# Kernel tuning notes

Hardware: AMD Instinct MI355X
Metric: run time of the kernel (lower is better)

## Reference

```python
import jax, jax.numpy as jnp
import numpy as np

TWO_PI = 2.0 * np.pi
DT = 0.01            # self.dt buffer
COE_D, COE_M = 2, 8  # interp_degree, interp_mesh_size (per dim) for coe fitters
NL_D, NL_M = 4, 40   # nonlinear fitter degree / mesh_size
NL_A, NL_B = -15.0, 15.0  # nonlinear_interp_mesh_bound


def lagrange_basis(t, d):
    """Degree-d Lagrange basis at local coord t in [0,1]; returns [..., d+1]."""
    nodes = jnp.arange(d + 1, dtype=t.dtype) / d
    basis = []
    for j in range(d + 1):
        L = jnp.ones_like(t)
        for k in range(d + 1):
            if k != j:
                L = L * (t - nodes[k]) / (nodes[j] - nodes[k])
        basis.append(L)
    return jnp.stack(basis, axis=-1)


def interp_cells(x, a, b, m, d):
    """Map x to (cell index [..,], basis values [.., d+1]) on an m-cell mesh over [a,b]."""
    s = (x - a) / (b - a) * m
    cell = jnp.clip(jnp.floor(s), 0, m - 1)
    t = s - cell  # allows extrapolation outside [a,b] via edge cells
    return cell.astype(jnp.int32), lagrange_basis(t, d)


def nonlinear_interp(w, x):
    """1D piecewise-Lagrange fitter applied elementwise (nonlinearfitter)."""
    cell, L = interp_cells(x, NL_A, NL_B, NL_M, NL_D)
    idx = cell[..., None] * NL_D + jnp.arange(NL_D + 1)
    return jnp.sum(w[idx] * L, axis=-1)


def coe_fields(ws, xy):
    """2D tensor-product Lagrange interp on fixed inputs xy -> [C,H,W] coef fields."""
    c0, L0 = interp_cells(xy[..., 0], 0.0, TWO_PI, COE_M, COE_D)
    c1, L1 = interp_cells(xy[..., 1], 0.0, TWO_PI, COE_M, COE_D)
    i0 = c0[..., None] * COE_D + jnp.arange(COE_D + 1)   # [H,W,d+1]
    i1 = c1[..., None] * COE_D + jnp.arange(COE_D + 1)
    wloc = ws[:, i0[..., :, None], i1[..., None, :]]     # [C,H,W,d+1,d+1]
    return jnp.einsum('chwij,hwi,hwj->chw', wloc, L0, L1)


def conv_same(u, k):
    """u: [B,H,W], k: [N,1,kh,kw] -> [B,N,H,W] with zero (Dirichlet) padding."""
    return jax.lax.conv_general_dilated(u[:, None], k, (1, 1), 'SAME',
                                        dimension_numbers=('NCHW', 'OIHW', 'NCHW'))


def setup_inputs() -> dict:
    key = jax.random.key(0)
    ks = jax.random.split(key, 5)
    B, H, W, K, N = 16, 512, 512, 5, 6
    init = jax.random.normal(ks[0], (B, H, W), jnp.float32)
    delta = jnp.zeros((1, 1, K, K), jnp.float32).at[0, 0, K // 2, K // 2].set(1.0)
    idkernel = delta + 0.01 * jax.random.normal(ks[1], (1, 1, K, K), jnp.float32)
    fdkernel = 0.1 * jax.random.normal(ks[2], (N, 1, K, K), jnp.float32)
    M = COE_M * COE_D + 1
    coe_w = 0.1 * jax.random.normal(ks[3], (N - 1, M, M), jnp.float32)
    nl_w = 0.1 * jax.random.normal(ks[4], (NL_M * NL_D + 1,), jnp.float32)
    gx = jnp.linspace(0.0, TWO_PI, H, endpoint=False).astype(jnp.float32)
    xy = jnp.stack(jnp.meshgrid(gx, gx, indexing='ij'), axis=-1)  # [H,W,2]
    return {"init": init, "idkernel": idkernel, "fdkernel": fdkernel,
            "coe_w": coe_w, "nl_w": nl_w, "xy": xy, "stepnum": 8}


def reference(init, idkernel, fdkernel, coe_w, nl_w, xy, stepnum):
    # coefficient fields are evaluated once (fixed xy), as in the torch forward
    coe = coe_fields(coe_w, xy)[None]  # [1, N-1, H, W], broadcasts over batch

    def step(u, _):
        uid = conv_same(u, idkernel)[:, 0]           # [B,H,W]
        ufd = conv_same(u, fdkernel)                 # [B,N,H,W]
        un = uid + DT * ((coe * ufd[:, 1:]).sum(axis=1)
                         + nonlinear_interp(nl_w, ufd[:, 0]))
        return un, None

    u, _ = jax.lax.scan(step, init, None, length=stepnum)
    return u
```

## Files before the change

### kernel.cpp

```cpp
#include <hip/hip_runtime.h>

typedef float f2 __attribute__((ext_vector_type(2)));

static constexpr int HH = 512;
static constexpr int WW = 512;
static constexpr int NB = 16;
static constexpr float DT_F = 0.01f;
static constexpr float TWO_PI_F = 6.283185307179586f;
static constexpr int STEPS = 8;

static constexpr int TW = 64;
static constexpr int TH = 16;
static constexpr int LW = TW + 4;
static constexpr int LH = TH + 4;

__device__ const float NLM[5][5] = {
    {1.0f,      -25.0f/3.0f,   70.0f/3.0f,  -80.0f/3.0f,   32.0f/3.0f},
    {0.0f,       16.0f,      -208.0f/3.0f,   96.0f,      -128.0f/3.0f},
    {0.0f,      -12.0f,        76.0f,      -128.0f,        64.0f},
    {0.0f,   16.0f/3.0f,    -112.0f/3.0f,  224.0f/3.0f, -128.0f/3.0f},
    {0.0f,      -1.0f,       22.0f/3.0f,   -16.0f,        32.0f/3.0f},
};

__device__ __forceinline__ void pkfma_s(f2& acc, f2 w, f2 u) {
    asm("v_pk_fma_f32 %0, %1, %2, %0" : "+v"(acc) : "s"(w), "v"(u));
}
__device__ __forceinline__ void pkfma_v(f2& acc, f2 a, f2 b) {
    asm("v_pk_fma_f32 %0, %1, %2, %0" : "+v"(acc) : "v"(a), "v"(b));
}

__global__ __launch_bounds__(256) void coe_kernel(const float* __restrict__ coe_w,
                                                  const float* __restrict__ xy,
                                                  float* __restrict__ coe)
{
    __shared__ float sw[5 * 17 * 17];
    for (int i = threadIdx.x; i < 5 * 17 * 17; i += 256) sw[i] = coe_w[i];
    __syncthreads();

    int p = blockIdx.x * 256 + threadIdx.x;
    if (p >= HH * WW) return;

    float x0 = xy[2 * p + 0];
    float x1 = xy[2 * p + 1];

    float s0 = x0 / TWO_PI_F * 8.0f;
    float c0f = fminf(fmaxf(floorf(s0), 0.0f), 7.0f);
    float t0 = s0 - c0f;
    int i0 = 2 * (int)c0f;

    float s1 = x1 / TWO_PI_F * 8.0f;
    float c1f = fminf(fmaxf(floorf(s1), 0.0f), 7.0f);
    float t1 = s1 - c1f;
    int i1 = 2 * (int)c1f;

    float L0[3], L1[3];
    L0[0] = (t0 - 0.5f) * (t0 - 1.0f) * 2.0f;
    L0[1] = t0 * (t0 - 1.0f) * -4.0f;
    L0[2] = t0 * (t0 - 0.5f) * 2.0f;
    L1[0] = (t1 - 0.5f) * (t1 - 1.0f) * 2.0f;
    L1[1] = t1 * (t1 - 1.0f) * -4.0f;
    L1[2] = t1 * (t1 - 0.5f) * 2.0f;

    #pragma unroll
    for (int c = 0; c < 5; ++c) {
        float acc = 0.0f;
        #pragma unroll
        for (int i = 0; i < 3; ++i) {
            #pragma unroll
            for (int j = 0; j < 3; ++j) {
                acc = fmaf(sw[c * 289 + (i0 + i) * 17 + (i1 + j)], L0[i] * L1[j], acc);
            }
        }
        coe[c * HH * WW + p] = acc;
    }
}

__global__ __launch_bounds__(256) void step_kernel(
    const float* __restrict__ uin,
    float* __restrict__ uout,
    const float* __restrict__ kid,
    const float* __restrict__ kfd,
    const float* __restrict__ nlw,
    const float* __restrict__ coe)
{
    __shared__ float su[LH][LW];
    __shared__ float snlp[40 * 8];

    const int tid = threadIdx.x;
    const int bx = blockIdx.x & 7;
    const int by = (blockIdx.x >> 3) & 31;
    const int b  = blockIdx.x >> 8;
    const int col0 = bx * TW;
    const int row0 = by * TH;
    const float* ub = uin + b * (HH * WW);

    if (tid < 200) {
        const int c = tid / 5;
        const int m = tid - 5 * c;
        float a = nlw[4 * c + 0] * NLM[0][m];
        a = fmaf(nlw[4 * c + 1], NLM[1][m], a);
        a = fmaf(nlw[4 * c + 2], NLM[2][m], a);
        a = fmaf(nlw[4 * c + 3], NLM[3][m], a);
        a = fmaf(nlw[4 * c + 4], NLM[4][m], a);
        snlp[c * 8 + m] = a;
    }

    for (int it = tid; it < LH * 18; it += 256) {
        const int lr = it / 18;
        const int j  = it - lr * 18;
        const int gr = row0 - 2 + lr;
        const int gc = col0 - 4 + 4 * j;
        float4 v = make_float4(0.f, 0.f, 0.f, 0.f);
        if (gr >= 0 && gr < HH && gc >= 0 && gc + 3 < WW)
            v = *reinterpret_cast<const float4*>(ub + gr * WW + gc);
        if (j == 0) {
            *reinterpret_cast<float2*>(&su[lr][0]) = make_float2(v.z, v.w);
        } else if (j == 17) {
            *reinterpret_cast<float2*>(&su[lr][66]) = make_float2(v.x, v.y);
        } else {
            const int lc = 4 * j - 2;
            *reinterpret_cast<float2*>(&su[lr][lc])     = make_float2(v.x, v.y);
            *reinterpret_cast<float2*>(&su[lr][lc + 2]) = make_float2(v.z, v.w);
        }
    }
    __syncthreads();

    const int t16 = tid & 15;
    const int tyr = tid >> 4;
    const int c4  = t16 * 4;

    f2 accid2[2];
    f2 accf2[6][2];
    accid2[0] = (f2){0.f, 0.f}; accid2[1] = (f2){0.f, 0.f};
    #pragma unroll
    for (int n = 0; n < 6; ++n) {
        accf2[n][0] = (f2){0.f, 0.f};
        accf2[n][1] = (f2){0.f, 0.f};
    }

    #pragma unroll
    for (int dy = 0; dy < 5; ++dy) {
        const float4 w0 = *reinterpret_cast<const float4*>(&su[tyr + dy][c4]);
        const float4 w1 = *reinterpret_cast<const float4*>(&su[tyr + dy][c4 + 4]);
        const f2 r01 = (f2){w0.x, w0.y};
        const f2 r23 = (f2){w0.z, w0.w};
        const f2 r45 = (f2){w1.x, w1.y};
        const f2 r67 = (f2){w1.z, w1.w};
        const f2 r12 = (f2){w0.y, w0.z};
        const f2 r34 = (f2){w0.w, w1.x};
        const f2 r56 = (f2){w1.y, w1.z};

        #define CONV_DX(DX, PL, PH)                                          \
        {                                                                     \
            const int o = dy * 5 + (DX);                                      \
            f2 wv;                                                            \
            wv.x = kid[o];       wv.y = wv.x;                                 \
            pkfma_s(accid2[0],   wv, PL); pkfma_s(accid2[1],   wv, PH);       \
            wv.x = kfd[o];       wv.y = wv.x;                                 \
            pkfma_s(accf2[0][0], wv, PL); pkfma_s(accf2[0][1], wv, PH);       \
            wv.x = kfd[25 + o];  wv.y = wv.x;                                 \
            pkfma_s(accf2[1][0], wv, PL); pkfma_s(accf2[1][1], wv, PH);       \
            wv.x = kfd[50 + o];  wv.y = wv.x;                                 \
            pkfma_s(accf2[2][0], wv, PL); pkfma_s(accf2[2][1], wv, PH);       \
            wv.x = kfd[75 + o];  wv.y = wv.x;                                 \
            pkfma_s(accf2[3][0], wv, PL); pkfma_s(accf2[3][1], wv, PH);       \
            wv.x = kfd[100 + o]; wv.y = wv.x;                                 \
            pkfma_s(accf2[4][0], wv, PL); pkfma_s(accf2[4][1], wv, PH);       \
            wv.x = kfd[125 + o]; wv.y = wv.x;                                 \
            pkfma_s(accf2[5][0], wv, PL); pkfma_s(accf2[5][1], wv, PH);       \
        }
        CONV_DX(0, r01, r23)
        CONV_DX(1, r12, r34)
        CONV_DX(2, r23, r45)
        CONV_DX(3, r34, r56)
        CONV_DX(4, r45, r67)
        #undef CONV_DX
    }

    const int p = (row0 + tyr) * WW + col0 + c4;

    f2 cs2[2];
    cs2[0] = (f2){0.f, 0.f}; cs2[1] = (f2){0.f, 0.f};
    #pragma unroll
    for (int n = 0; n < 5; ++n) {
        const float4 cv = *reinterpret_cast<const float4*>(&coe[n * HH * WW + p]);
        const f2 c01 = (f2){cv.x, cv.y};
        const f2 c23 = (f2){cv.z, cv.w};
        pkfma_v(cs2[0], c01, accf2[n + 1][0]);
        pkfma_v(cs2[1], c23, accf2[n + 1][1]);
    }

    const float xs[4]  = {accf2[0][0].x, accf2[0][0].y, accf2[0][1].x, accf2[0][1].y};
    const float csv[4] = {cs2[0].x, cs2[0].y, cs2[1].x, cs2[1].y};
    const float idv[4] = {accid2[0].x, accid2[0].y, accid2[1].x, accid2[1].y};

    float outv[4];
    #pragma unroll
    for (int k = 0; k < 4; ++k) {
        const float x = xs[k];
        const float sc = fmaf(x, 4.0f / 3.0f, 20.0f);
        const float cf = fminf(fmaxf(floorf(sc), 0.0f), 39.0f);
        const float t = sc - cf;
        const int base = (int)cf * 8;
        const float4 cm = *reinterpret_cast<const float4*>(&snlp[base]);
        const float cm4 = snlp[base + 4];
        float r = fmaf(cm4, t, cm.w);
        r = fmaf(r, t, cm.z);
        r = fmaf(r, t, cm.y);
        r = fmaf(r, t, cm.x);
        outv[k] = fmaf(DT_F, csv[k] + r, idv[k]);
    }

    *reinterpret_cast<float4*>(&uout[b * (HH * WW) + p]) =
        make_float4(outv[0], outv[1], outv[2], outv[3]);
}

extern "C" void kernel_launch(void* const* d_in, const int* in_sizes, int n_in,
                              void* d_out, int out_size, void* d_ws, size_t ws_size,
                              hipStream_t stream)
{
    const float* init = (const float*)d_in[0];
    const float* idk  = (const float*)d_in[1];
    const float* fdk  = (const float*)d_in[2];
    const float* coew = (const float*)d_in[3];
    const float* nlw  = (const float*)d_in[4];
    const float* xy   = (const float*)d_in[5];

    float* ws  = (float*)d_ws;
    float* coe = ws;
    float* uA  = coe + 5 * HH * WW;
    float* uB  = uA + NB * HH * WW;

    coe_kernel<<<(HH * WW + 255) / 256, 256, 0, stream>>>(coew, xy, coe);

    const int nblk = NB * (HH / TH) * (WW / TW);
    const float* src = init;
    for (int s = 0; s < STEPS; ++s) {
        float* dst = (s == STEPS - 1) ? (float*)d_out : ((s & 1) ? uB : uA);
        step_kernel<<<nblk, 256, 0, stream>>>(src, dst, idk, fdk, nlw, coe);
        src = dst;
    }
}
```

Measured before the change: 186.5 us.

## Fuse two time steps per kernel via halo recompute in shared memory

```diff
diff --git a/kernel.cpp b/kernel.cpp
--- a/kernel.cpp
+++ b/kernel.cpp
@@ -4,15 +4,17 @@
 
 static constexpr int HH = 512;
 static constexpr int WW = 512;
+static constexpr int HW = HH * WW;
 static constexpr int NB = 16;
 static constexpr float DT_F = 0.01f;
 static constexpr float TWO_PI_F = 6.283185307179586f;
-static constexpr int STEPS = 8;
 
 static constexpr int TW = 64;
 static constexpr int TH = 16;
-static constexpr int LW = TW + 4;
-static constexpr int LH = TH + 4;
+static constexpr int SW = TW + 8;
+static constexpr int SH = TH + 8;
+static constexpr int MW = TW + 4;
+static constexpr int MH = TH + 4;
 
 __device__ const float NLM[5][5] = {
     {1.0f,      -25.0f/3.0f,   70.0f/3.0f,  -80.0f/3.0f,   32.0f/3.0f},
@@ -29,119 +31,22 @@
     asm("v_pk_fma_f32 %0, %1, %2, %0" : "+v"(acc) : "v"(a), "v"(b));
 }
 
-__global__ __launch_bounds__(256) void coe_kernel(const float* __restrict__ coe_w,
-                                                  const float* __restrict__ xy,
-                                                  float* __restrict__ coe)
-{
-    __shared__ float sw[5 * 17 * 17];
-    for (int i = threadIdx.x; i < 5 * 17 * 17; i += 256) sw[i] = coe_w[i];
-    __syncthreads();
-
-    int p = blockIdx.x * 256 + threadIdx.x;
-    if (p >= HH * WW) return;
-
-    float x0 = xy[2 * p + 0];
-    float x1 = xy[2 * p + 1];
-
-    float s0 = x0 / TWO_PI_F * 8.0f;
-    float c0f = fminf(fmaxf(floorf(s0), 0.0f), 7.0f);
-    float t0 = s0 - c0f;
-    int i0 = 2 * (int)c0f;
-
-    float s1 = x1 / TWO_PI_F * 8.0f;
-    float c1f = fminf(fmaxf(floorf(s1), 0.0f), 7.0f);
-    float t1 = s1 - c1f;
-    int i1 = 2 * (int)c1f;
-
-    float L0[3], L1[3];
-    L0[0] = (t0 - 0.5f) * (t0 - 1.0f) * 2.0f;
-    L0[1] = t0 * (t0 - 1.0f) * -4.0f;
-    L0[2] = t0 * (t0 - 0.5f) * 2.0f;
-    L1[0] = (t1 - 0.5f) * (t1 - 1.0f) * 2.0f;
-    L1[1] = t1 * (t1 - 1.0f) * -4.0f;
-    L1[2] = t1 * (t1 - 0.5f) * 2.0f;
-
-    #pragma unroll
-    for (int c = 0; c < 5; ++c) {
-        float acc = 0.0f;
-        #pragma unroll
-        for (int i = 0; i < 3; ++i) {
-            #pragma unroll
-            for (int j = 0; j < 3; ++j) {
-                acc = fmaf(sw[c * 289 + (i0 + i) * 17 + (i1 + j)], L0[i] * L1[j], acc);
-            }
-        }
-        coe[c * HH * WW + p] = acc;
-    }
-}
-
-__global__ __launch_bounds__(256) void step_kernel(
-    const float* __restrict__ uin,
-    float* __restrict__ uout,
-    const float* __restrict__ kid,
-    const float* __restrict__ kfd,
-    const float* __restrict__ nlw,
-    const float* __restrict__ coe)
-{
-    __shared__ float su[LH][LW];
-    __shared__ float snlp[40 * 8];
-
-    const int tid = threadIdx.x;
-    const int bx = blockIdx.x & 7;
-    const int by = (blockIdx.x >> 3) & 31;
-    const int b  = blockIdx.x >> 8;
-    const int col0 = bx * TW;
-    const int row0 = by * TH;
-    const float* ub = uin + b * (HH * WW);
-
-    if (tid < 200) {
-        const int c = tid / 5;
-        const int m = tid - 5 * c;
-        float a = nlw[4 * c + 0] * NLM[0][m];
-        a = fmaf(nlw[4 * c + 1], NLM[1][m], a);
-        a = fmaf(nlw[4 * c + 2], NLM[2][m], a);
-        a = fmaf(nlw[4 * c + 3], NLM[3][m], a);
-        a = fmaf(nlw[4 * c + 4], NLM[4][m], a);
-        snlp[c * 8 + m] = a;
-    }
-
-    for (int it = tid; it < LH * 18; it += 256) {
-        const int lr = it / 18;
-        const int j  = it - lr * 18;
-        const int gr = row0 - 2 + lr;
-        const int gc = col0 - 4 + 4 * j;
-        float4 v = make_float4(0.f, 0.f, 0.f, 0.f);
-        if (gr >= 0 && gr < HH && gc >= 0 && gc + 3 < WW)
-            v = *reinterpret_cast<const float4*>(ub + gr * WW + gc);
-        if (j == 0) {
-            *reinterpret_cast<float2*>(&su[lr][0]) = make_float2(v.z, v.w);
-        } else if (j == 17) {
-            *reinterpret_cast<float2*>(&su[lr][66]) = make_float2(v.x, v.y);
-        } else {
-            const int lc = 4 * j - 2;
-            *reinterpret_cast<float2*>(&su[lr][lc])     = make_float2(v.x, v.y);
-            *reinterpret_cast<float2*>(&su[lr][lc + 2]) = make_float2(v.z, v.w);
-        }
-    }
-    __syncthreads();
-
-    const int t16 = tid & 15;
-    const int tyr = tid >> 4;
-    const int c4  = t16 * 4;
-
-    f2 accid2[2];
-    f2 accf2[6][2];
+template<int STRIDE>
+__device__ __forceinline__ void conv7(const float* base,
+                                      const float* __restrict__ kid,
+                                      const float* __restrict__ kfd,
+                                      f2 accid2[2], f2 accf2[6][2])
+{
     accid2[0] = (f2){0.f, 0.f}; accid2[1] = (f2){0.f, 0.f};
     #pragma unroll
     for (int n = 0; n < 6; ++n) {
         accf2[n][0] = (f2){0.f, 0.f};
         accf2[n][1] = (f2){0.f, 0.f};
     }
-
     #pragma unroll
     for (int dy = 0; dy < 5; ++dy) {
-        const float4 w0 = *reinterpret_cast<const float4*>(&su[tyr + dy][c4]);
-        const float4 w1 = *reinterpret_cast<const float4*>(&su[tyr + dy][c4 + 4]);
+        const float4 w0 = *reinterpret_cast<const float4*>(base + dy * STRIDE);
+        const float4 w1 = *reinterpret_cast<const float4*>(base + dy * STRIDE + 4);
         const f2 r01 = (f2){w0.x, w0.y};
         const f2 r23 = (f2){w0.z, w0.w};
         const f2 r45 = (f2){w1.x, w1.y};
@@ -176,43 +81,190 @@
         CONV_DX(4, r45, r67)
         #undef CONV_DX
     }
-
-    const int p = (row0 + tyr) * WW + col0 + c4;
-
-    f2 cs2[2];
-    cs2[0] = (f2){0.f, 0.f}; cs2[1] = (f2){0.f, 0.f};
+}
+
+__device__ __forceinline__ float nl_eval(const float* __restrict__ snlp, float x)
+{
+    const float sc = fmaf(x, 4.0f / 3.0f, 20.0f);
+    const float cf = fminf(fmaxf(floorf(sc), 0.0f), 39.0f);
+    const float t = sc - cf;
+    const int base = (int)cf * 8;
+    const float4 cm = *reinterpret_cast<const float4*>(&snlp[base]);
+    const float cm4 = snlp[base + 4];
+    float r = fmaf(cm4, t, cm.w);
+    r = fmaf(r, t, cm.z);
+    r = fmaf(r, t, cm.y);
+    r = fmaf(r, t, cm.x);
+    return r;
+}
+
+__global__ __launch_bounds__(256) void coe_kernel(const float* __restrict__ coe_w,
+                                                  const float* __restrict__ xy,
+                                                  float* __restrict__ coe)
+{
+    __shared__ float sw[5 * 17 * 17];
+    for (int i = threadIdx.x; i < 5 * 17 * 17; i += 256) sw[i] = coe_w[i];
+    __syncthreads();
+
+    int p = blockIdx.x * 256 + threadIdx.x;
+    if (p >= HW) return;
+
+    float x0 = xy[2 * p + 0];
+    float x1 = xy[2 * p + 1];
+
+    float s0 = x0 / TWO_PI_F * 8.0f;
+    float c0f = fminf(fmaxf(floorf(s0), 0.0f), 7.0f);
+    float t0 = s0 - c0f;
+    int i0 = 2 * (int)c0f;
+
+    float s1 = x1 / TWO_PI_F * 8.0f;
+    float c1f = fminf(fmaxf(floorf(s1), 0.0f), 7.0f);
+    float t1 = s1 - c1f;
+    int i1 = 2 * (int)c1f;
+
+    float L0[3], L1[3];
+    L0[0] = (t0 - 0.5f) * (t0 - 1.0f) * 2.0f;
+    L0[1] = t0 * (t0 - 1.0f) * -4.0f;
+    L0[2] = t0 * (t0 - 0.5f) * 2.0f;
+    L1[0] = (t1 - 0.5f) * (t1 - 1.0f) * 2.0f;
+    L1[1] = t1 * (t1 - 1.0f) * -4.0f;
+    L1[2] = t1 * (t1 - 0.5f) * 2.0f;
+
     #pragma unroll
-    for (int n = 0; n < 5; ++n) {
-        const float4 cv = *reinterpret_cast<const float4*>(&coe[n * HH * WW + p]);
-        const f2 c01 = (f2){cv.x, cv.y};
-        const f2 c23 = (f2){cv.z, cv.w};
-        pkfma_v(cs2[0], c01, accf2[n + 1][0]);
-        pkfma_v(cs2[1], c23, accf2[n + 1][1]);
-    }
-
-    const float xs[4]  = {accf2[0][0].x, accf2[0][0].y, accf2[0][1].x, accf2[0][1].y};
-    const float csv[4] = {cs2[0].x, cs2[0].y, cs2[1].x, cs2[1].y};
-    const float idv[4] = {accid2[0].x, accid2[0].y, accid2[1].x, accid2[1].y};
-
-    float outv[4];
-    #pragma unroll
-    for (int k = 0; k < 4; ++k) {
-        const float x = xs[k];
-        const float sc = fmaf(x, 4.0f / 3.0f, 20.0f);
-        const float cf = fminf(fmaxf(floorf(sc), 0.0f), 39.0f);
-        const float t = sc - cf;
-        const int base = (int)cf * 8;
-        const float4 cm = *reinterpret_cast<const float4*>(&snlp[base]);
-        const float cm4 = snlp[base + 4];
-        float r = fmaf(cm4, t, cm.w);
-        r = fmaf(r, t, cm.z);
-        r = fmaf(r, t, cm.y);
-        r = fmaf(r, t, cm.x);
-        outv[k] = fmaf(DT_F, csv[k] + r, idv[k]);
-    }
-
-    *reinterpret_cast<float4*>(&uout[b * (HH * WW) + p]) =
-        make_float4(outv[0], outv[1], outv[2], outv[3]);
+    for (int c = 0; c < 5; ++c) {
+        float acc = 0.0f;
+        #pragma unroll
+        for (int i = 0; i < 3; ++i) {
+            #pragma unroll
+            for (int j = 0; j < 3; ++j) {
+                acc = fmaf(sw[c * 289 + (i0 + i) * 17 + (i1 + j)], L0[i] * L1[j], acc);
+            }
+        }
+        coe[c * HW + p] = acc;
+    }
+}
+
+__global__ __launch_bounds__(256) void fused2_kernel(
+    const float* __restrict__ uin,
+    float* __restrict__ uout,
+    const float* __restrict__ kid,
+    const float* __restrict__ kfd,
+    const float* __restrict__ nlw,
+    const float* __restrict__ coe)
+{
+    __shared__ float su[SH][SW];
+    __shared__ float smid[MH][MW];
+    __shared__ float snlp[40 * 8];
+
+    const int tid = threadIdx.x;
+    const int bx = blockIdx.x & 7;
+    const int by = (blockIdx.x >> 3) & 31;
+    const int b  = blockIdx.x >> 8;
+    const int col0 = bx * TW;
+    const int row0 = by * TH;
+    const float* ub = uin + b * HW;
+
+    if (tid < 200) {
+        const int c = tid / 5;
+        const int m = tid - 5 * c;
+        float a = nlw[4 * c + 0] * NLM[0][m];
+        a = fmaf(nlw[4 * c + 1], NLM[1][m], a);
+        a = fmaf(nlw[4 * c + 2], NLM[2][m], a);
+        a = fmaf(nlw[4 * c + 3], NLM[3][m], a);
+        a = fmaf(nlw[4 * c + 4], NLM[4][m], a);
+        snlp[c * 8 + m] = a;
+    }
+
+    for (int it = tid; it < SH * 18; it += 256) {
+        const int lr = it / 18;
+        const int j  = it - lr * 18;
+        const int gr = row0 - 4 + lr;
+        const int gc = col0 - 4 + 4 * j;
+        float4 v = make_float4(0.f, 0.f, 0.f, 0.f);
+        if (gr >= 0 && gr < HH && gc >= 0 && gc + 3 < WW)
+            v = *reinterpret_cast<const float4*>(ub + gr * WW + gc);
+        *reinterpret_cast<float4*>(&su[lr][4 * j]) = v;
+    }
+    __syncthreads();
+
+    #pragma unroll 1
+    for (int iter = 0; iter < 2; ++iter) {
+        const int q = iter * 256 + tid;
+        if (q >= MH * 17) break;
+        const int r1 = q / 17;
+        const int m0 = 4 * (q - 17 * r1);
+
+        f2 accid2[2], accf2[6][2];
+        conv7<SW>(&su[r1][m0], kid, kfd, accid2, accf2);
+
+        const int grow = row0 - 2 + r1;
+        const int gc0  = col0 - 2 + m0;
+        const bool rowok = (grow >= 0) & (grow < HH);
+
+        const int pr = rowok ? grow * WW : 0;
+        const int pA = min(max(pr + gc0, 0), HW - 2);
+        const int pB = min(max(pr + gc0 + 2, 0), HW - 2);
+        f2 cs2[2];
+        cs2[0] = (f2){0.f, 0.f}; cs2[1] = (f2){0.f, 0.f};
+        #pragma unroll
+        for (int n = 0; n < 5; ++n) {
+            const f2 cA = *reinterpret_cast<const f2*>(&coe[n * HW + pA]);
+            const f2 cB = *reinterpret_cast<const f2*>(&coe[n * HW + pB]);
+            pkfma_v(cs2[0], cA, accf2[n + 1][0]);
+            pkfma_v(cs2[1], cB, accf2[n + 1][1]);
+        }
+
+        const float xs[4]  = {accf2[0][0].x, accf2[0][0].y, accf2[0][1].x, accf2[0][1].y};
+        const float csv[4] = {cs2[0].x, cs2[0].y, cs2[1].x, cs2[1].y};
+        const float idv[4] = {accid2[0].x, accid2[0].y, accid2[1].x, accid2[1].y};
+
+        float outv[4];
+        #pragma unroll
+        for (int k = 0; k < 4; ++k) {
+            const float nl = nl_eval(snlp, xs[k]);
+            const int gck = gc0 + k;
+            const bool ok = rowok & (gck >= 0) & (gck < WW);
+            outv[k] = ok ? fmaf(DT_F, csv[k] + nl, idv[k]) : 0.0f;
+        }
+        *reinterpret_cast<float4*>(&smid[r1][m0]) =
+            make_float4(outv[0], outv[1], outv[2], outv[3]);
+    }
+    __syncthreads();
+
+    {
+        const int t16 = tid & 15;
+        const int r   = tid >> 4;
+        const int c4  = 4 * t16;
+
+        f2 accid2[2], accf2[6][2];
+        conv7<MW>(&smid[r][c4], kid, kfd, accid2, accf2);
+
+        const int p = (row0 + r) * WW + col0 + c4;
+
+        f2 cs2[2];
+        cs2[0] = (f2){0.f, 0.f}; cs2[1] = (f2){0.f, 0.f};
+        #pragma unroll
+        for (int n = 0; n < 5; ++n) {
+            const float4 cv = *reinterpret_cast<const float4*>(&coe[n * HW + p]);
+            const f2 c01 = (f2){cv.x, cv.y};
+            const f2 c23 = (f2){cv.z, cv.w};
+            pkfma_v(cs2[0], c01, accf2[n + 1][0]);
+            pkfma_v(cs2[1], c23, accf2[n + 1][1]);
+        }
+
+        const float xs[4]  = {accf2[0][0].x, accf2[0][0].y, accf2[0][1].x, accf2[0][1].y};
+        const float csv[4] = {cs2[0].x, cs2[0].y, cs2[1].x, cs2[1].y};
+        const float idv[4] = {accid2[0].x, accid2[0].y, accid2[1].x, accid2[1].y};
+
+        float outv[4];
+        #pragma unroll
+        for (int k = 0; k < 4; ++k) {
+            const float nl = nl_eval(snlp, xs[k]);
+            outv[k] = fmaf(DT_F, csv[k] + nl, idv[k]);
+        }
+        *reinterpret_cast<float4*>(&uout[b * HW + p]) =
+            make_float4(outv[0], outv[1], outv[2], outv[3]);
+    }
 }
 
 extern "C" void kernel_launch(void* const* d_in, const int* in_sizes, int n_in,
@@ -228,16 +280,14 @@
 
     float* ws  = (float*)d_ws;
     float* coe = ws;
-    float* uA  = coe + 5 * HH * WW;
-    float* uB  = uA + NB * HH * WW;
-
-    coe_kernel<<<(HH * WW + 255) / 256, 256, 0, stream>>>(coew, xy, coe);
+    float* uA  = coe + 5 * HW;
+    float* uB  = uA + NB * HW;
+
+    coe_kernel<<<(HW + 255) / 256, 256, 0, stream>>>(coew, xy, coe);
 
     const int nblk = NB * (HH / TH) * (WW / TW);
-    const float* src = init;
-    for (int s = 0; s < STEPS; ++s) {
-        float* dst = (s == STEPS - 1) ? (float*)d_out : ((s & 1) ? uB : uA);
-        step_kernel<<<nblk, 256, 0, stream>>>(src, dst, idk, fdk, nlw, coe);
-        src = dst;
-    }
-}
+    fused2_kernel<<<nblk, 256, 0, stream>>>(init, uA, idk, fdk, nlw, coe);
+    fused2_kernel<<<nblk, 256, 0, stream>>>(uA, uB, idk, fdk, nlw, coe);
+    fused2_kernel<<<nblk, 256, 0, stream>>>(uB, uA, idk, fdk, nlw, coe);
+    fused2_kernel<<<nblk, 256, 0, stream>>>(uA, (float*)d_out, idk, fdk, nlw, coe);
+}
```

After: 201.4 us. 8.0% more time.

## Fold coefficient fields into per-pixel effective kernels and loop batches per block

Applied to the files above, without the earlier changes.

```diff
diff --git a/kernel.cpp b/kernel.cpp
--- a/kernel.cpp
+++ b/kernel.cpp
@@ -4,15 +4,16 @@
 
 static constexpr int HH = 512;
 static constexpr int WW = 512;
+static constexpr int HW = HH * WW;
 static constexpr int NB = 16;
 static constexpr float DT_F = 0.01f;
 static constexpr float TWO_PI_F = 6.283185307179586f;
-static constexpr int STEPS = 8;
-
-static constexpr int TW = 64;
+
+static constexpr int TW = 32;
 static constexpr int TH = 16;
-static constexpr int LW = TW + 4;
-static constexpr int LH = TH + 4;
+static constexpr int SWx = TW + 4;
+static constexpr int SHx = TH + 4;
+static constexpr int NTASK = SHx * 10 * 2;
 
 __device__ const float NLM[5][5] = {
     {1.0f,      -25.0f/3.0f,   70.0f/3.0f,  -80.0f/3.0f,   32.0f/3.0f},
@@ -29,16 +30,32 @@
     asm("v_pk_fma_f32 %0, %1, %2, %0" : "+v"(acc) : "v"(a), "v"(b));
 }
 
-__global__ __launch_bounds__(256) void coe_kernel(const float* __restrict__ coe_w,
-                                                  const float* __restrict__ xy,
-                                                  float* __restrict__ coe)
+__device__ __forceinline__ float nl_eval(const float* __restrict__ snlp, float x)
+{
+    const float sc = fmaf(x, 4.0f / 3.0f, 20.0f);
+    const float cf = fminf(fmaxf(floorf(sc), 0.0f), 39.0f);
+    const float t = sc - cf;
+    const int base = (int)cf * 8;
+    const float4 cm = *reinterpret_cast<const float4*>(&snlp[base]);
+    const float cm4 = snlp[base + 4];
+    float r = fmaf(cm4, t, cm.w);
+    r = fmaf(r, t, cm.z);
+    r = fmaf(r, t, cm.y);
+    r = fmaf(r, t, cm.x);
+    return r;
+}
+
+__global__ __launch_bounds__(256) void keff_kernel(const float* __restrict__ coe_w,
+                                                   const float* __restrict__ xy,
+                                                   const float* __restrict__ fdk,
+                                                   float* __restrict__ keff)
 {
     __shared__ float sw[5 * 17 * 17];
     for (int i = threadIdx.x; i < 5 * 17 * 17; i += 256) sw[i] = coe_w[i];
     __syncthreads();
 
     int p = blockIdx.x * 256 + threadIdx.x;
-    if (p >= HH * WW) return;
+    if (p >= HW) return;
 
     float x0 = xy[2 * p + 0];
     float x1 = xy[2 * p + 1];
@@ -61,6 +78,7 @@
     L1[1] = t1 * (t1 - 1.0f) * -4.0f;
     L1[2] = t1 * (t1 - 0.5f) * 2.0f;
 
+    float coe[5];
     #pragma unroll
     for (int c = 0; c < 5; ++c) {
         float acc = 0.0f;
@@ -71,7 +89,44 @@
                 acc = fmaf(sw[c * 289 + (i0 + i) * 17 + (i1 + j)], L0[i] * L1[j], acc);
             }
         }
-        coe[c * HH * WW + p] = acc;
+        coe[c] = acc;
+    }
+
+    #pragma unroll
+    for (int t = 0; t < 25; ++t) {
+        float v = coe[0] * fdk[25 + t];
+        v = fmaf(coe[1], fdk[50 + t], v);
+        v = fmaf(coe[2], fdk[75 + t], v);
+        v = fmaf(coe[3], fdk[100 + t], v);
+        v = fmaf(coe[4], fdk[125 + t], v);
+        keff[t * HW + p] = v;
+    }
+}
+
+__device__ __forceinline__ float4 ld_u(const float* __restrict__ u,
+                                       int row0, int col0, int idx)
+{
+    const int lr = idx / 10;
+    const int j  = idx - 10 * lr;
+    const int gr = row0 - 2 + lr;
+    const int gc = col0 - 4 + 4 * j;
+    float4 v = make_float4(0.f, 0.f, 0.f, 0.f);
+    if (gr >= 0 && gr < HH && gc >= 0 && gc + 3 < WW)
+        v = *reinterpret_cast<const float4*>(u + gr * WW + gc);
+    return v;
+}
+__device__ __forceinline__ void st_u(float* __restrict__ su2, int idx, float4 v)
+{
+    const int lr = idx / 10;
+    const int j  = idx - 10 * lr;
+    float* row = su2 + lr * SWx;
+    if (j == 0) {
+        *reinterpret_cast<float2*>(row) = make_float2(v.z, v.w);
+    } else if (j == 9) {
+        *reinterpret_cast<float2*>(row + 34) = make_float2(v.x, v.y);
+    } else {
+        *reinterpret_cast<float2*>(row + 4 * j - 2) = make_float2(v.x, v.y);
+        *reinterpret_cast<float2*>(row + 4 * j)     = make_float2(v.z, v.w);
     }
 }
 
@@ -81,18 +136,23 @@
     const float* __restrict__ kid,
     const float* __restrict__ kfd,
     const float* __restrict__ nlw,
-    const float* __restrict__ coe)
-{
-    __shared__ float su[LH][LW];
+    const float* __restrict__ keff)
+{
+    __shared__ float su[2][2][SHx * SWx];
     __shared__ float snlp[40 * 8];
 
     const int tid = threadIdx.x;
-    const int bx = blockIdx.x & 7;
-    const int by = (blockIdx.x >> 3) & 31;
-    const int b  = blockIdx.x >> 8;
+    const int bx = blockIdx.x & 15;
+    const int by = blockIdx.x >> 4;
     const int col0 = bx * TW;
     const int row0 = by * TH;
-    const float* ub = uin + b * (HH * WW);
+
+    const int bh  = tid >> 7;
+    const int q   = tid & 127;
+    const int t8  = q & 7;
+    const int tyr = q >> 3;
+    const int c4  = 4 * t8;
+    const int p0  = (row0 + tyr) * WW + col0 + c4;
 
     if (tid < 200) {
         const int c = tid / 5;
@@ -105,114 +165,90 @@
         snlp[c * 8 + m] = a;
     }
 
-    for (int it = tid; it < LH * 18; it += 256) {
-        const int lr = it / 18;
-        const int j  = it - lr * 18;
-        const int gr = row0 - 2 + lr;
-        const int gc = col0 - 4 + 4 * j;
-        float4 v = make_float4(0.f, 0.f, 0.f, 0.f);
-        if (gr >= 0 && gr < HH && gc >= 0 && gc + 3 < WW)
-            v = *reinterpret_cast<const float4*>(ub + gr * WW + gc);
-        if (j == 0) {
-            *reinterpret_cast<float2*>(&su[lr][0]) = make_float2(v.z, v.w);
-        } else if (j == 17) {
-            *reinterpret_cast<float2*>(&su[lr][66]) = make_float2(v.x, v.y);
-        } else {
-            const int lc = 4 * j - 2;
-            *reinterpret_cast<float2*>(&su[lr][lc])     = make_float2(v.x, v.y);
-            *reinterpret_cast<float2*>(&su[lr][lc + 2]) = make_float2(v.z, v.w);
-        }
-    }
-    __syncthreads();
-
-    const int t16 = tid & 15;
-    const int tyr = tid >> 4;
-    const int c4  = t16 * 4;
-
-    f2 accid2[2];
-    f2 accf2[6][2];
-    accid2[0] = (f2){0.f, 0.f}; accid2[1] = (f2){0.f, 0.f};
+    f2 ke[25][2];
     #pragma unroll
-    for (int n = 0; n < 6; ++n) {
-        accf2[n][0] = (f2){0.f, 0.f};
-        accf2[n][1] = (f2){0.f, 0.f};
-    }
-
-    #pragma unroll
-    for (int dy = 0; dy < 5; ++dy) {
-        const float4 w0 = *reinterpret_cast<const float4*>(&su[tyr + dy][c4]);
-        const float4 w1 = *reinterpret_cast<const float4*>(&su[tyr + dy][c4 + 4]);
-        const f2 r01 = (f2){w0.x, w0.y};
-        const f2 r23 = (f2){w0.z, w0.w};
-        const f2 r45 = (f2){w1.x, w1.y};
-        const f2 r67 = (f2){w1.z, w1.w};
-        const f2 r12 = (f2){w0.y, w0.z};
-        const f2 r34 = (f2){w0.w, w1.x};
-        const f2 r56 = (f2){w1.y, w1.z};
-
-        #define CONV_DX(DX, PL, PH)                                          \
-        {                                                                     \
-            const int o = dy * 5 + (DX);                                      \
-            f2 wv;                                                            \
-            wv.x = kid[o];       wv.y = wv.x;                                 \
-            pkfma_s(accid2[0],   wv, PL); pkfma_s(accid2[1],   wv, PH);       \
-            wv.x = kfd[o];       wv.y = wv.x;                                 \
-            pkfma_s(accf2[0][0], wv, PL); pkfma_s(accf2[0][1], wv, PH);       \
-            wv.x = kfd[25 + o];  wv.y = wv.x;                                 \
-            pkfma_s(accf2[1][0], wv, PL); pkfma_s(accf2[1][1], wv, PH);       \
-            wv.x = kfd[50 + o];  wv.y = wv.x;                                 \
-            pkfma_s(accf2[2][0], wv, PL); pkfma_s(accf2[2][1], wv, PH);       \
-            wv.x = kfd[75 + o];  wv.y = wv.x;                                 \
-            pkfma_s(accf2[3][0], wv, PL); pkfma_s(accf2[3][1], wv, PH);       \
-            wv.x = kfd[100 + o]; wv.y = wv.x;                                 \
-            pkfma_s(accf2[4][0], wv, PL); pkfma_s(accf2[4][1], wv, PH);       \
-            wv.x = kfd[125 + o]; wv.y = wv.x;                                 \
-            pkfma_s(accf2[5][0], wv, PL); pkfma_s(accf2[5][1], wv, PH);       \
-        }
-        CONV_DX(0, r01, r23)
-        CONV_DX(1, r12, r34)
-        CONV_DX(2, r23, r45)
-        CONV_DX(3, r34, r56)
-        CONV_DX(4, r45, r67)
-        #undef CONV_DX
-    }
-
-    const int p = (row0 + tyr) * WW + col0 + c4;
-
-    f2 cs2[2];
-    cs2[0] = (f2){0.f, 0.f}; cs2[1] = (f2){0.f, 0.f};
-    #pragma unroll
-    for (int n = 0; n < 5; ++n) {
-        const float4 cv = *reinterpret_cast<const float4*>(&coe[n * HH * WW + p]);
-        const f2 c01 = (f2){cv.x, cv.y};
-        const f2 c23 = (f2){cv.z, cv.w};
-        pkfma_v(cs2[0], c01, accf2[n + 1][0]);
-        pkfma_v(cs2[1], c23, accf2[n + 1][1]);
-    }
-
-    const float xs[4]  = {accf2[0][0].x, accf2[0][0].y, accf2[0][1].x, accf2[0][1].y};
-    const float csv[4] = {cs2[0].x, cs2[0].y, cs2[1].x, cs2[1].y};
-    const float idv[4] = {accid2[0].x, accid2[0].y, accid2[1].x, accid2[1].y};
-
-    float outv[4];
-    #pragma unroll
-    for (int k = 0; k < 4; ++k) {
-        const float x = xs[k];
-        const float sc = fmaf(x, 4.0f / 3.0f, 20.0f);
-        const float cf = fminf(fmaxf(floorf(sc), 0.0f), 39.0f);
-        const float t = sc - cf;
-        const int base = (int)cf * 8;
-        const float4 cm = *reinterpret_cast<const float4*>(&snlp[base]);
-        const float cm4 = snlp[base + 4];
-        float r = fmaf(cm4, t, cm.w);
-        r = fmaf(r, t, cm.z);
-        r = fmaf(r, t, cm.y);
-        r = fmaf(r, t, cm.x);
-        outv[k] = fmaf(DT_F, csv[k] + r, idv[k]);
-    }
-
-    *reinterpret_cast<float4*>(&uout[b * (HH * WW) + p]) =
-        make_float4(outv[0], outv[1], outv[2], outv[3]);
+    for (int t = 0; t < 25; ++t) {
+        const float4 kv = *reinterpret_cast<const float4*>(keff + t * HW + p0);
+        ke[t][0] = (f2){kv.x, kv.y};
+        ke[t][1] = (f2){kv.z, kv.w};
+    }
+
+    const int task0 = tid;
+    const int task1 = tid + 256;
+    const bool has1 = task1 < NTASK;
+    const int t0h = task0 >= 200;
+    const int i0x = task0 - 200 * t0h;
+    const int t1h = 1;
+    const int i1x = task1 - 200;
+
+    float4 s0 = ld_u(uin + (size_t)(t0h * 8 + 0) * HW, row0, col0, i0x);
+    float4 s1 = has1 ? ld_u(uin + (size_t)(t1h * 8 + 0) * HW, row0, col0, i1x)
+                     : make_float4(0.f, 0.f, 0.f, 0.f);
+    st_u(su[0][t0h], i0x, s0);
+    if (has1) st_u(su[0][t1h], i1x, s1);
+
+    for (int b = 0; b < 8; ++b) {
+        const int buf = b & 1;
+        if (b < 7) {
+            s0 = ld_u(uin + (size_t)(t0h * 8 + b + 1) * HW, row0, col0, i0x);
+            if (has1) s1 = ld_u(uin + (size_t)(t1h * 8 + b + 1) * HW, row0, col0, i1x);
+        }
+        __syncthreads();
+
+        const float* base = su[buf][bh] + tyr * SWx + c4;
+        f2 aid[2], af0[2], aef[2];
+        aid[0] = (f2){0.f, 0.f}; aid[1] = (f2){0.f, 0.f};
+        af0[0] = (f2){0.f, 0.f}; af0[1] = (f2){0.f, 0.f};
+        aef[0] = (f2){0.f, 0.f}; aef[1] = (f2){0.f, 0.f};
+
+        #pragma unroll
+        for (int dy = 0; dy < 5; ++dy) {
+            const float4 w0 = *reinterpret_cast<const float4*>(base + dy * SWx);
+            const float4 w1 = *reinterpret_cast<const float4*>(base + dy * SWx + 4);
+            const f2 r01 = (f2){w0.x, w0.y};
+            const f2 r23 = (f2){w0.z, w0.w};
+            const f2 r45 = (f2){w1.x, w1.y};
+            const f2 r67 = (f2){w1.z, w1.w};
+            const f2 r12 = (f2){w0.y, w0.z};
+            const f2 r34 = (f2){w0.w, w1.x};
+            const f2 r56 = (f2){w1.y, w1.z};
+
+            #define CONV_DX(DX, PL, PH)                                      \
+            {                                                                 \
+                const int o = dy * 5 + (DX);                                  \
+                f2 wv;                                                        \
+                wv.x = kid[o]; wv.y = wv.x;                                   \
+                pkfma_s(aid[0], wv, PL); pkfma_s(aid[1], wv, PH);             \
+                wv.x = kfd[o]; wv.y = wv.x;                                   \
+                pkfma_s(af0[0], wv, PL); pkfma_s(af0[1], wv, PH);             \
+                pkfma_v(aef[0], ke[o][0], PL);                                \
+                pkfma_v(aef[1], ke[o][1], PH);                                \
+            }
+            CONV_DX(0, r01, r23)
+            CONV_DX(1, r12, r34)
+            CONV_DX(2, r23, r45)
+            CONV_DX(3, r34, r56)
+            CONV_DX(4, r45, r67)
+            #undef CONV_DX
+        }
+
+        const float xs[4]  = {af0[0].x, af0[0].y, af0[1].x, af0[1].y};
+        const float efv[4] = {aef[0].x, aef[0].y, aef[1].x, aef[1].y};
+        const float idv[4] = {aid[0].x, aid[0].y, aid[1].x, aid[1].y};
+        float outv[4];
+        #pragma unroll
+        for (int k = 0; k < 4; ++k) {
+            const float nl = nl_eval(snlp, xs[k]);
+            outv[k] = fmaf(DT_F, efv[k] + nl, idv[k]);
+        }
+        *reinterpret_cast<float4*>(uout + (size_t)(b + 8 * bh) * HW + p0) =
+            make_float4(outv[0], outv[1], outv[2], outv[3]);
+
+        if (b < 7) {
+            st_u(su[buf ^ 1][t0h], i0x, s0);
+            if (has1) st_u(su[buf ^ 1][t1h], i1x, s1);
+        }
+    }
 }
 
 extern "C" void kernel_launch(void* const* d_in, const int* in_sizes, int n_in,
@@ -226,18 +262,17 @@
     const float* nlw  = (const float*)d_in[4];
     const float* xy   = (const float*)d_in[5];
 
-    float* ws  = (float*)d_ws;
-    float* coe = ws;
-    float* uA  = coe + 5 * HH * WW;
-    float* uB  = uA + NB * HH * WW;
-
-    coe_kernel<<<(HH * WW + 255) / 256, 256, 0, stream>>>(coew, xy, coe);
-
-    const int nblk = NB * (HH / TH) * (WW / TW);
+    float* keff = (float*)d_ws;
+    float* uA   = keff + 25 * HW;
+    float* outp = (float*)d_out;
+
+    keff_kernel<<<(HW + 255) / 256, 256, 0, stream>>>(coew, xy, fdk, keff);
+
+    const int nblk = (WW / TW) * (HH / TH);
     const float* src = init;
-    for (int s = 0; s < STEPS; ++s) {
-        float* dst = (s == STEPS - 1) ? (float*)d_out : ((s & 1) ? uB : uA);
-        step_kernel<<<nblk, 256, 0, stream>>>(src, dst, idk, fdk, nlw, coe);
+    for (int s = 0; s < 8; ++s) {
+        float* dst = (s & 1) ? outp : uA;
+        step_kernel<<<nblk, 256, 0, stream>>>(src, dst, idk, fdk, nlw, keff);
         src = dst;
     }
 }
```

Result: no change. 186.2 us (-0.2%).
